# Performance work log

Measured on AMD Instinct MI355X. Metric: run time of the kernel, lower is better.

The kernel has to match this reference:

```python
import jax, jax.numpy as jnp
import numpy as np

B, S, H, NH, HD = 2, 2048, 2048, 16, 128
E, TOPK, I = 8, 2, 2048
EPS = 1e-5
ROPE_THETA = 10000.0


def setup_inputs() -> dict:
    key = jax.random.key(0)
    ks = jax.random.split(key, 11)
    s = 0.02
    return {
        "hidden_states": jax.random.normal(ks[0], (B, S, H), jnp.float32),
        "position_ids": jnp.broadcast_to(jnp.arange(S, dtype=jnp.int32), (B, S)),
        "rms1_w": jnp.ones((H,), jnp.float32),
        "rms2_w": jnp.ones((H,), jnp.float32),
        "q_w": jax.random.normal(ks[1], (H, H), jnp.float32) * s,
        "k_w": jax.random.normal(ks[2], (H, H), jnp.float32) * s,
        "v_w": jax.random.normal(ks[3], (H, H), jnp.float32) * s,
        "o_w": jax.random.normal(ks[4], (H, H), jnp.float32) * s,
        "router_w": jax.random.normal(ks[5], (H, E), jnp.float32) * s,
        "w1": jax.random.normal(ks[6], (E, H, I), jnp.float32) * s,
        "w2": jax.random.normal(ks[7], (E, I, H), jnp.float32) * s,
        "w3": jax.random.normal(ks[8], (E, H, I), jnp.float32) * s,
    }


def rmsnorm(x, w):
    var = jnp.mean(x * x, axis=-1, keepdims=True)
    return (x * jax.lax.rsqrt(var + EPS)) * w


def rope(x, pos):
    # x: [B,S,NH,HD], pos: [B,S]
    half = HD // 2
    inv_freq = 1.0 / (ROPE_THETA ** (jnp.arange(0, half, dtype=jnp.float32) / half))
    ang = pos.astype(jnp.float32)[..., None] * inv_freq  # [B,S,half]
    cos = jnp.cos(ang)[:, :, None, :]
    sin = jnp.sin(ang)[:, :, None, :]
    x1, x2 = x[..., :half], x[..., half:]
    return jnp.concatenate([x1 * cos - x2 * sin, x2 * cos + x1 * sin], axis=-1)


def attention(x, pos, q_w, k_w, v_w, o_w):
    q = (x @ q_w).reshape(B, S, NH, HD)
    k = (x @ k_w).reshape(B, S, NH, HD)
    v = (x @ v_w).reshape(B, S, NH, HD)
    q = rope(q, pos)
    k = rope(k, pos)
    scores = jnp.einsum("bqhd,bkhd->bhqk", q, k) / np.sqrt(HD).astype(np.float32)
    causal = jnp.tril(jnp.ones((S, S), bool))
    scores = jnp.where(causal, scores, jnp.finfo(scores.dtype).min)
    probs = jax.nn.softmax(scores, axis=-1)
    ctx = jnp.einsum("bhqk,bkhd->bqhd", probs, v).reshape(B, S, H)
    return ctx @ o_w


def moe(x, router_w, w1, w2, w3):
    t = x.reshape(B * S, H)
    probs = jax.nn.softmax(t @ router_w, axis=-1)  # [T,E]
    top_v, top_i = jax.lax.top_k(probs, TOPK)
    top_v = top_v / jnp.sum(top_v, axis=-1, keepdims=True)
    T = B * S
    coeff = jnp.zeros((T, E), x.dtype).at[jnp.arange(T)[:, None], top_i].set(top_v)
    y = jnp.zeros((T, H), x.dtype)
    for e in range(E):  # fixed small expert loop
        h = jax.nn.silu(t @ w1[e]) * (t @ w3[e])
        y = y + coeff[:, e:e + 1] * (h @ w2[e])
    return y.reshape(B, S, H)


def reference(hidden_states, position_ids, rms1_w, rms2_w, q_w, k_w, v_w, o_w,
              router_w, w1, w2, w3):
    residual = hidden_states
    h = rmsnorm(hidden_states, rms1_w).astype(hidden_states.dtype)
    h = attention(h, position_ids, q_w, k_w, v_w, o_w)
    h = residual + h
    residual = h
    h = rmsnorm(h, rms2_w).astype(h.dtype)
    h = moe(h, router_w, w1, w2, w3)
    return residual + h
```

## Files before the change

kernel.cpp:

```cpp
#include <hip/hip_runtime.h>
#include <hip/hip_bf16.h>

constexpr int CB   = 2;
constexpr int CS   = 2048;
constexpr int CH   = 2048;
constexpr int CNH  = 16;
constexpr int CHD  = 128;
constexpr int CE   = 8;
constexpr int CI   = 2048;
constexpr int CT   = CB * CS;
constexpr int CQKV = 3 * CH;

typedef __attribute__((ext_vector_type(8))) short short8;
typedef __attribute__((ext_vector_type(4))) float float4v;
typedef __attribute__((ext_vector_type(4))) unsigned short ushort4v;
typedef unsigned int uint32;

__device__ __forceinline__ float bf2f(unsigned short u) {
    union { unsigned int i; float f; } x; x.i = ((unsigned int)u) << 16; return x.f;
}
__device__ __forceinline__ unsigned short f2bf(float f) {
    union { float f; unsigned int i; } x; x.f = f;
    unsigned int r = x.i + 0x7fffu + ((x.i >> 16) & 1u);
    return (unsigned short)(r >> 16);
}
__device__ __forceinline__ uint32 packpair(uint32 r0, uint32 r1) {
    return __builtin_amdgcn_perm(r1, r0, 0x07060302u);
}
__device__ __forceinline__ uint32 rnebits(float f) {
    uint32 u = __float_as_uint(f);
    return u + 0x7fffu + ((u >> 16) & 1u);
}
__device__ __forceinline__ void split2(float f0, float f1, uint32& h, uint32& l) {
    uint32 r0 = rnebits(f0), r1 = rnebits(f1);
    h = packpair(r0, r1);
    float d0 = f0 - __uint_as_float(r0 & 0xffff0000u);
    float d1 = f1 - __uint_as_float(r1 & 0xffff0000u);
    l = packpair(rnebits(d0), rnebits(d1));
}
__device__ __forceinline__ void rne16_store(const float* fv, unsigned short* dst) {
    uint32 h[8];
    #pragma unroll
    for (int p = 0; p < 8; p++) h[p] = packpair(rnebits(fv[2 * p]), rnebits(fv[2 * p + 1]));
    ((uint4*)dst)[0] = make_uint4(h[0], h[1], h[2], h[3]);
    ((uint4*)dst)[1] = make_uint4(h[4], h[5], h[6], h[7]);
}

__global__ __launch_bounds__(256) void rmsnorm_k(const float* __restrict__ x,
                                                 const float* __restrict__ w,
                                                 unsigned short* __restrict__ o1,
                                                 unsigned short* __restrict__ o2) {
    const int row = blockIdx.x;
    const float* xr = x + (size_t)row * CH;
    const int base = threadIdx.x * 8;
    float4 v0 = *(const float4*)(xr + base);
    float4 v1 = *(const float4*)(xr + base + 4);
    float ss = v0.x*v0.x + v0.y*v0.y + v0.z*v0.z + v0.w*v0.w
             + v1.x*v1.x + v1.y*v1.y + v1.z*v1.z + v1.w*v1.w;
    #pragma unroll
    for (int o = 1; o < 64; o <<= 1) ss += __shfl_xor(ss, o);
    __shared__ float ps[4];
    if ((threadIdx.x & 63) == 0) ps[threadIdx.x >> 6] = ss;
    __syncthreads();
    const float scale = rsqrtf((ps[0] + ps[1] + ps[2] + ps[3]) / (float)CH + 1e-5f);
    float4 w0 = *(const float4*)(w + base);
    float4 w1 = *(const float4*)(w + base + 4);
    float r[8] = {v0.x * scale * w0.x, v0.y * scale * w0.y, v0.z * scale * w0.z, v0.w * scale * w0.w,
                  v1.x * scale * w1.x, v1.y * scale * w1.y, v1.z * scale * w1.z, v1.w * scale * w1.w};
    uint32 h[4], l[4];
    #pragma unroll
    for (int p = 0; p < 4; p++) split2(r[2 * p], r[2 * p + 1], h[p], l[p]);
    *(uint4*)(o1 + (size_t)row * CH + base) = make_uint4(h[0], h[1], h[2], h[3]);
    *(uint4*)(o2 + (size_t)row * CH + base) = make_uint4(l[0], l[1], l[2], l[3]);
}

__global__ __launch_bounds__(256) void rmsrouter_k(const float* __restrict__ x,
                                                   const float* __restrict__ w,
                                                   const float* __restrict__ rw,
                                                   unsigned short* __restrict__ h2,
                                                   int* __restrict__ cnt,
                                                   int* __restrict__ tok,
                                                   float* __restrict__ gate) {
    const int row = blockIdx.x;
    const float* xr = x + (size_t)row * CH;
    const int base = threadIdx.x * 8;
    float4 v0 = *(const float4*)(xr + base);
    float4 v1 = *(const float4*)(xr + base + 4);
    float ss = v0.x*v0.x + v0.y*v0.y + v0.z*v0.z + v0.w*v0.w
             + v1.x*v1.x + v1.y*v1.y + v1.z*v1.z + v1.w*v1.w;
    #pragma unroll
    for (int o = 1; o < 64; o <<= 1) ss += __shfl_xor(ss, o);
    __shared__ float ps[4];
    __shared__ double dacc[4][8];
    const int wave = threadIdx.x >> 6, lane = threadIdx.x & 63;
    if (lane == 0) ps[wave] = ss;
    __syncthreads();
    const float scale = rsqrtf((ps[0] + ps[1] + ps[2] + ps[3]) / (float)CH + 1e-5f);
    float4 w0 = *(const float4*)(w + base);
    float4 w1 = *(const float4*)(w + base + 4);
    float r[8] = {v0.x * scale * w0.x, v0.y * scale * w0.y, v0.z * scale * w0.z, v0.w * scale * w0.w,
                  v1.x * scale * w1.x, v1.y * scale * w1.y, v1.z * scale * w1.z, v1.w * scale * w1.w};
    rne16_store(r, h2 + (size_t)row * CH + base);
    const float vv[8] = {v0.x, v0.y, v0.z, v0.w, v1.x, v1.y, v1.z, v1.w};
    const float ww[8] = {w0.x, w0.y, w0.z, w0.w, w1.x, w1.y, w1.z, w1.w};
    double acc[8] = {0, 0, 0, 0, 0, 0, 0, 0};
    #pragma unroll
    for (int jj = 0; jj < 8; jj++) {
        const double xn = (double)vv[jj] * (double)ww[jj];
        const float* rr = rw + (size_t)(base + jj) * CE;
        #pragma unroll
        for (int e = 0; e < 8; e++) acc[e] += xn * (double)rr[e];
    }
    #pragma unroll
    for (int e = 0; e < 8; e++) {
        #pragma unroll
        for (int o = 1; o < 64; o <<= 1) acc[e] += __shfl_xor(acc[e], o);
    }
    if (lane == 0) {
        #pragma unroll
        for (int e = 0; e < 8; e++) dacc[wave][e] = acc[e];
    }
    __syncthreads();
    if (threadIdx.x == 0) {
        double a[8];
        #pragma unroll
        for (int e = 0; e < 8; e++) a[e] = dacc[0][e] + dacc[1][e] + dacc[2][e] + dacc[3][e];
        int e0 = 0;
        #pragma unroll
        for (int e = 1; e < 8; e++) if (a[e] > a[e0]) e0 = e;
        int e1 = (e0 == 0) ? 1 : 0;
        #pragma unroll
        for (int e = 0; e < 8; e++) if (e != e0 && a[e] > a[e1]) e1 = e;
        const double dl = (double)scale * (a[e1] - a[e0]);
        const double p1r = exp(dl);
        const float g0 = (float)(1.0 / (1.0 + p1r));
        const float g1 = (float)(p1r / (1.0 + p1r));
        int pos0 = atomicAdd(&cnt[e0], 1);
        tok[e0 * 4096 + pos0] = row; gate[e0 * 4096 + pos0] = g0;
        int pos1 = atomicAdd(&cnt[e1], 1);
        tok[e1 * 4096 + pos1] = row; gate[e1 * 4096 + pos1] = g1;
    }
}

__global__ void rope_tab_k(float2* __restrict__ tab) {
    int i = blockIdx.x * 256 + threadIdx.x;
    int p = i >> 6, j = i & 63;
    double inv = pow(10000.0, -(double)j / 64.0);
    float invf = (float)inv;
    float angf = (float)p * invf;
    double da = (double)angf;
    tab[i] = make_float2((float)cos(da), (float)sin(da));
}

__global__ __launch_bounds__(256) void rope_k(unsigned short* __restrict__ qh,
                                              unsigned short* __restrict__ ql,
                                              const int* __restrict__ pos,
                                              const float2* __restrict__ tab) {
    int i = blockIdx.x * 256 + threadIdx.x;
    if (i >= CT * CNH * 8) return;
    int t = i >> 7, r = i & 127, hh = r >> 3, jo = (r & 7) << 3;
    const float2* tp = tab + (size_t)pos[t] * 64 + jo;
    float4 tc0 = ((const float4*)tp)[0];
    float4 tc1 = ((const float4*)tp)[1];
    float4 tc2 = ((const float4*)tp)[2];
    float4 tc3 = ((const float4*)tp)[3];
    float cx[8] = {tc0.x, tc0.z, tc1.x, tc1.z, tc2.x, tc2.z, tc3.x, tc3.z};
    float cy[8] = {tc0.y, tc0.w, tc1.y, tc1.w, tc2.y, tc2.w, tc3.y, tc3.w};
    const size_t off = (size_t)t * CQKV + hh * CHD + jo;
    #pragma unroll
    for (int s = 0; s < 2; s++) {
        unsigned short* hp = qh + off + s * CH;
        unsigned short* lp = ql + off + s * CH;
        short8 x1h = *(short8*)hp,        x1l = *(short8*)lp;
        short8 x2h = *(short8*)(hp + 64), x2l = *(short8*)(lp + 64);
        const unsigned short* p1h = (const unsigned short*)&x1h;
        const unsigned short* p1l = (const unsigned short*)&x1l;
        const unsigned short* p2h = (const unsigned short*)&x2h;
        const unsigned short* p2l = (const unsigned short*)&x2l;
        short8 y1h, y1l, y2h, y2l;
        unsigned short* q1h = (unsigned short*)&y1h;
        unsigned short* q1l = (unsigned short*)&y1l;
        unsigned short* q2h = (unsigned short*)&y2h;
        unsigned short* q2l = (unsigned short*)&y2l;
        #pragma unroll
        for (int jj = 0; jj < 8; jj++) {
            const float x1 = bf2f(p1h[jj]) + bf2f(p1l[jj]);
            const float x2 = bf2f(p2h[jj]) + bf2f(p2l[jj]);
            const float yy1 = x1 * cx[jj] - x2 * cy[jj];
            const float yy2 = x2 * cx[jj] + x1 * cy[jj];
            const uint32 r1 = rnebits(yy1), r2 = rnebits(yy2);
            q1h[jj] = (unsigned short)(r1 >> 16);
            q2h[jj] = (unsigned short)(r2 >> 16);
            q1l[jj] = f2bf(yy1 - __uint_as_float(r1 & 0xffff0000u));
            q2l[jj] = f2bf(yy2 - __uint_as_float(r2 & 0xffff0000u));
        }
        *(short8*)hp        = y1h;
        *(short8*)(hp + 64) = y2h;
        *(short8*)lp        = y1l;
        *(short8*)(lp + 64) = y2l;
    }
}

template<int NMAT>
__global__ __launch_bounds__(256) void conv_k(const float* __restrict__ S0,
                                              const float* __restrict__ S1,
                                              unsigned short* __restrict__ D) {
    __shared__ float t[64][65];
    const int n0 = blockIdx.x * 64, k0 = blockIdx.y * 64, e = blockIdx.z;
    const size_t esrc = (size_t)e * 2048 * 2048;
    const int cc = threadIdx.x & 63, r4 = threadIdx.x >> 6;
    const int nl = threadIdx.x >> 2, q = threadIdx.x & 3;
    #pragma unroll
    for (int s = 0; s < NMAT; s++) {
        const float* S = s ? S1 : S0;
        __syncthreads();
        #pragma unroll
        for (int j = 0; j < 16; j++) {
            const int row = j * 4 + r4;
            t[cc][row] = S[esrc + (size_t)(k0 + row) * 2048 + n0 + cc];
        }
        __syncthreads();
        const int orow = (NMAT == 2) ? (2 * (n0 + nl) + s) : (n0 + nl);
        unsigned short* dp = D + (size_t)e * (NMAT * 2048) * 2048 + (size_t)orow * 2048 + k0 + q * 16;
        float fv[16];
        #pragma unroll
        for (int j = 0; j < 16; j++) fv[j] = t[nl][q * 16 + j];
        rne16_store(fv, dp);
    }
}

template<int NMAT>
__global__ __launch_bounds__(256) void convs_k(const float* __restrict__ S0,
                                               const float* __restrict__ S1,
                                               const float* __restrict__ S2,
                                               unsigned short* __restrict__ Dh,
                                               unsigned short* __restrict__ Dl) {
    __shared__ float t[64][65];
    const int n0 = blockIdx.x * 64, k0 = blockIdx.y * 64, z = blockIdx.z;
    const float* S = S0;
    if (NMAT == 3) S = (z == 0) ? S0 : ((z == 1) ? S1 : S2);
    const int cc = threadIdx.x & 63, r4 = threadIdx.x >> 6;
    #pragma unroll
    for (int j = 0; j < 16; j++) {
        const int row = j * 4 + r4;
        t[cc][row] = S[(size_t)(k0 + row) * 2048 + n0 + cc];
    }
    __syncthreads();
    const int nl = threadIdx.x >> 2, q = threadIdx.x & 3;
    float fv[16];
    #pragma unroll
    for (int j = 0; j < 16; j++) fv[j] = t[nl][q * 16 + j];
    uint32 h[8], l[8];
    #pragma unroll
    for (int p = 0; p < 8; p++) split2(fv[2 * p], fv[2 * p + 1], h[p], l[p]);
    const size_t off = (size_t)(z * 2048 + n0 + nl) * 2048 + k0 + q * 16;
    ((uint4*)(Dh + off))[0] = make_uint4(h[0], h[1], h[2], h[3]);
    ((uint4*)(Dh + off))[1] = make_uint4(h[4], h[5], h[6], h[7]);
    ((uint4*)(Dl + off))[0] = make_uint4(l[0], l[1], l[2], l[3]);
    ((uint4*)(Dl + off))[1] = make_uint4(l[4], l[5], l[6], l[7]);
}

template<int MODE>
__global__ __launch_bounds__(256) void sgemm_k(
    const unsigned short* __restrict__ Ahg, const unsigned short* __restrict__ Alg, int lda,
    const unsigned short* __restrict__ Bhg, const unsigned short* __restrict__ Blg, int K,
    unsigned short* __restrict__ Ch, unsigned short* __restrict__ Cl,
    float* __restrict__ Cf, int ldc,
    const float* __restrict__ resid, float* __restrict__ C2) {
    __shared__ unsigned short AhS[128][40], AlS[128][40], BhS[128][40], BlS[128][40];
    const int mt = blockIdx.x, nt = blockIdx.y, tid = threadIdx.x;
    const int m0 = mt * 128;
    const int srow = tid >> 1, shalf = tid & 1;
    const unsigned short* ah = Ahg + (size_t)(m0 + srow) * lda + shalf * 16;
    const unsigned short* al = Alg + (size_t)(m0 + srow) * lda + shalf * 16;
    const unsigned short* bhp = Bhg + (size_t)(nt * 128 + srow) * K + shalf * 16;
    const unsigned short* blp = Blg + (size_t)(nt * 128 + srow) * K + shalf * 16;
    const int lane = tid & 63, lr = lane & 15, lg = lane >> 4;
    const int wr = (tid >> 7) & 1, wc = (tid >> 6) & 1;

    float4v acc[4][4];
    #pragma unroll
    for (int m = 0; m < 4; m++)
        #pragma unroll
        for (int n = 0; n < 4; n++) acc[m][n] = (float4v){0.f, 0.f, 0.f, 0.f};

    short8 cah0 = *(const short8*)(ah),      cah1 = *(const short8*)(ah + 8);
    short8 cal0 = *(const short8*)(al),      cal1 = *(const short8*)(al + 8);
    short8 cbh0 = *(const short8*)(bhp),     cbh1 = *(const short8*)(bhp + 8);
    short8 cbl0 = *(const short8*)(blp),     cbl1 = *(const short8*)(blp + 8);
    short8 nah0 = *(const short8*)(ah + 32), nah1 = *(const short8*)(ah + 40);
    short8 nal0 = *(const short8*)(al + 32), nal1 = *(const short8*)(al + 40);
    short8 nbh0 = *(const short8*)(bhp + 32), nbh1 = *(const short8*)(bhp + 40);
    short8 nbl0 = *(const short8*)(blp + 32), nbl1 = *(const short8*)(blp + 40);

    for (int k0 = 0; k0 < K; k0 += 32) {
        __syncthreads();
        *(short8*)(&AhS[srow][shalf * 16])     = cah0;
        *(short8*)(&AhS[srow][shalf * 16 + 8]) = cah1;
        *(short8*)(&AlS[srow][shalf * 16])     = cal0;
        *(short8*)(&AlS[srow][shalf * 16 + 8]) = cal1;
        *(short8*)(&BhS[srow][shalf * 16])     = cbh0;
        *(short8*)(&BhS[srow][shalf * 16 + 8]) = cbh1;
        *(short8*)(&BlS[srow][shalf * 16])     = cbl0;
        *(short8*)(&BlS[srow][shalf * 16 + 8]) = cbl1;
        cah0 = nah0; cah1 = nah1; cal0 = nal0; cal1 = nal1;
        cbh0 = nbh0; cbh1 = nbh1; cbl0 = nbl0; cbl1 = nbl1;
        if (k0 + 64 < K) {
            nah0 = *(const short8*)(ah + k0 + 64);  nah1 = *(const short8*)(ah + k0 + 72);
            nal0 = *(const short8*)(al + k0 + 64);  nal1 = *(const short8*)(al + k0 + 72);
            nbh0 = *(const short8*)(bhp + k0 + 64); nbh1 = *(const short8*)(bhp + k0 + 72);
            nbl0 = *(const short8*)(blp + k0 + 64); nbl1 = *(const short8*)(blp + k0 + 72);
        }
        __syncthreads();
        short8 fah[4], fal[4], fbh[4], fbl[4];
        #pragma unroll
        for (int m = 0; m < 4; m++) {
            fah[m] = *(const short8*)(&AhS[wr * 64 + m * 16 + lr][lg * 8]);
            fal[m] = *(const short8*)(&AlS[wr * 64 + m * 16 + lr][lg * 8]);
        }
        #pragma unroll
        for (int n = 0; n < 4; n++) {
            fbh[n] = *(const short8*)(&BhS[wc * 64 + n * 16 + lr][lg * 8]);
            fbl[n] = *(const short8*)(&BlS[wc * 64 + n * 16 + lr][lg * 8]);
        }
        #pragma unroll
        for (int n = 0; n < 4; n++)
            #pragma unroll
            for (int m = 0; m < 4; m++) {
                acc[m][n] = __builtin_amdgcn_mfma_f32_16x16x32_bf16(fal[m], fbh[n], acc[m][n], 0, 0, 0);
                acc[m][n] = __builtin_amdgcn_mfma_f32_16x16x32_bf16(fah[m], fbl[n], acc[m][n], 0, 0, 0);
                acc[m][n] = __builtin_amdgcn_mfma_f32_16x16x32_bf16(fah[m], fbh[n], acc[m][n], 0, 0, 0);
            }
    }
    #pragma unroll
    for (int m = 0; m < 4; m++) {
        const int rb = wr * 64 + m * 16 + lg * 4;
        #pragma unroll
        for (int n = 0; n < 4; n++) {
            const int ccol = nt * 128 + wc * 64 + n * 16 + lr;
            #pragma unroll
            for (int r = 0; r < 4; r++) {
                const size_t idx = (size_t)(m0 + rb + r) * ldc + ccol;
                if (MODE == 1) {
                    const float v = acc[m][n][r] + resid[idx];
                    Cf[idx] = v;
                    C2[idx] = v;
                } else {
                    const float v = acc[m][n][r];
                    uint32 rr = rnebits(v);
                    Ch[idx] = (unsigned short)(rr >> 16);
                    Cl[idx] = f2bf(v - __uint_as_float(rr & 0xffff0000u));
                }
            }
        }
    }
}

template<int MODE>
__global__ __launch_bounds__(256) void gemm_k(
    const unsigned short* __restrict__ A, int lda,
    const unsigned short* __restrict__ Bt, int K, int Ne,
    void* __restrict__ Cp, int ldc,
    const int* __restrict__ cnt, const int* __restrict__ tokl,
    const float* __restrict__ gatel, const int* __restrict__ pb) {
    __shared__ unsigned short As[128][40];
    __shared__ unsigned short Bs[128][40];
    const int nt = blockIdx.x, mt = blockIdx.y, e = blockIdx.z;
    const int m0 = mt * 128;
    const int c = cnt[e];
    if (m0 >= c) return;
    const int valid = (c - m0 < 128) ? (c - m0) : 128;
    const int tid = threadIdx.x;
    const int srow = tid >> 1, shalf = tid & 1;
    size_t gr;
    if (MODE == 2) {
        const int idx = m0 + (srow < valid ? srow : valid - 1);
        gr = (size_t)tokl[e * 4096 + idx];
    } else {
        const int rr = m0 + srow;
        gr = (size_t)(pb[e] + (rr < c ? rr : c - 1));
    }
    const unsigned short* a_src = A + gr * (size_t)lda + shalf * 16;
    const unsigned short* b_src = Bt + (size_t)e * Ne * K + (size_t)(nt * 128 + srow) * K + shalf * 16;
    const int lane = tid & 63, lr = lane & 15, lg = lane >> 4;
    const int wr = (tid >> 7) & 1, wc = (tid >> 6) & 1;

    float4v acc[4][4];
    #pragma unroll
    for (int m = 0; m < 4; m++)
        #pragma unroll
        for (int n = 0; n < 4; n++) acc[m][n] = (float4v){0.f, 0.f, 0.f, 0.f};

    short8 ca0 = *(const short8*)(a_src),      ca1 = *(const short8*)(a_src + 8);
    short8 cb0 = *(const short8*)(b_src),      cb1 = *(const short8*)(b_src + 8);
    short8 na0 = *(const short8*)(a_src + 32), na1 = *(const short8*)(a_src + 40);
    short8 nb0 = *(const short8*)(b_src + 32), nb1 = *(const short8*)(b_src + 40);

    for (int k0 = 0; k0 < K; k0 += 32) {
        __syncthreads();
        *(short8*)(&As[srow][shalf * 16])     = ca0;
        *(short8*)(&As[srow][shalf * 16 + 8]) = ca1;
        *(short8*)(&Bs[srow][shalf * 16])     = cb0;
        *(short8*)(&Bs[srow][shalf * 16 + 8]) = cb1;
        ca0 = na0; ca1 = na1; cb0 = nb0; cb1 = nb1;
        if (k0 + 64 < K) {
            na0 = *(const short8*)(a_src + k0 + 64);
            na1 = *(const short8*)(a_src + k0 + 72);
            nb0 = *(const short8*)(b_src + k0 + 64);
            nb1 = *(const short8*)(b_src + k0 + 72);
        }
        __syncthreads();
        short8 af[4], bf[4];
        #pragma unroll
        for (int m = 0; m < 4; m++) af[m] = *(const short8*)(&As[wr * 64 + m * 16 + lr][lg * 8]);
        #pragma unroll
        for (int n = 0; n < 4; n++) bf[n] = *(const short8*)(&Bs[wc * 64 + n * 16 + lr][lg * 8]);
        #pragma unroll
        for (int n = 0; n < 4; n++)
            #pragma unroll
            for (int m = 0; m < 4; m++)
                acc[m][n] = __builtin_amdgcn_mfma_f32_16x16x32_bf16(af[m], bf[n], acc[m][n], 0, 0, 0);
    }

    #pragma unroll
    for (int m = 0; m < 4; m++) {
        const int rb = wr * 64 + m * 16 + lg * 4;
        #pragma unroll
        for (int n = 0; n < 4; n++) {
            const int col = nt * 128 + wc * 64 + n * 16 + lr;
            #pragma unroll
            for (int r = 0; r < 4; r++) {
                const int row = rb + r;
                const float v = acc[m][n][r];
                if (MODE == 2) {
                    const float other = __shfl_xor(v, 1);
                    if (!(lr & 1) && row < valid) {
                        const float g1 = v, g3 = other;
                        const float hsw = (g1 / (1.f + __expf(-g1))) * g3;
                        ((unsigned short*)Cp)[(size_t)(pb[e] + m0 + row) * ldc + (col >> 1)] = f2bf(hsw);
                    }
                } else {
                    if (row < valid) {
                        const int t = tokl[e * 4096 + m0 + row];
                        const float g = gatel[e * 4096 + m0 + row];
                        atomicAdd(((float*)Cp) + (size_t)t * ldc + col, v * g);
                    }
                }
            }
        }
    }
}

__global__ __launch_bounds__(256) void attn_k(const unsigned short* __restrict__ qh,
                                              const unsigned short* __restrict__ ql,
                                              unsigned short* __restrict__ ch,
                                              unsigned short* __restrict__ cl) {
    __shared__ unsigned short Ksh[32][136], Ksl[32][136];
    __shared__ unsigned short Vth[128][40], Vtl[128][40];
    const int bid = blockIdx.x;
    const int xcd = bid & 7, jj = bid >> 3;
    const int bh  = xcd * 4 + (jj >> 5);
    const int qb  = 31 - (jj & 31);
    const int h   = bh & 15, b = bh >> 4;
    const int tid = threadIdx.x;
    const int wave = tid >> 6, lane = tid & 63, lr = lane & 15, lg = lane >> 4;
    const size_t tb = (size_t)b * CS;
    const int q0 = qb * 64 + wave * 16;

    short8 qfh[4], qfl[4];
    {
        const size_t off = (tb + q0 + lr) * CQKV + h * CHD;
        #pragma unroll
        for (int c = 0; c < 4; c++) {
            qfh[c] = *(const short8*)(qh + off + c * 32 + lg * 8);
            qfl[c] = *(const short8*)(ql + off + c * 32 + lg * 8);
        }
    }
    float4v o[8];
    #pragma unroll
    for (int d = 0; d < 8; d++) o[d] = (float4v){0.f, 0.f, 0.f, 0.f};
    float m = -1e30f, l = 0.f;
    const float scl = 0.08838834764831845f;
    const int ntiles = 2 * (qb + 1);
    const int kk = tid >> 3, slot = tid & 7;
    const int vd = tid & 127, vhalf = tid >> 7;

    short8 pkh0, pkh1, pkl0, pkl1;
    unsigned short pth[16], ptl[16];
    {
        const size_t koff = (tb + kk) * CQKV + CH + h * CHD + slot * 16;
        pkh0 = *(const short8*)(qh + koff);
        pkh1 = *(const short8*)(qh + koff + 8);
        pkl0 = *(const short8*)(ql + koff);
        pkl1 = *(const short8*)(ql + koff + 8);
        const size_t voff = (tb + vhalf * 16) * CQKV + 2 * CH + h * CHD + vd;
        #pragma unroll
        for (int j = 0; j < 16; j++) {
            pth[j] = qh[voff + (size_t)j * CQKV];
            ptl[j] = ql[voff + (size_t)j * CQKV];
        }
    }

    for (int kt = 0; kt < ntiles; ++kt) {
        const int kv0 = kt * 32;
        __syncthreads();
        *(short8*)(&Ksh[kk][slot * 16])     = pkh0;
        *(short8*)(&Ksh[kk][slot * 16 + 8]) = pkh1;
        *(short8*)(&Ksl[kk][slot * 16])     = pkl0;
        *(short8*)(&Ksl[kk][slot * 16 + 8]) = pkl1;
        #pragma unroll
        for (int p = 0; p < 2; p++) {
            *(ushort4v*)(&Vth[vd][vhalf * 16 + p * 8])     = *(ushort4v*)(&pth[p * 8]);
            *(ushort4v*)(&Vth[vd][vhalf * 16 + p * 8 + 4]) = *(ushort4v*)(&pth[p * 8 + 4]);
            *(ushort4v*)(&Vtl[vd][vhalf * 16 + p * 8])     = *(ushort4v*)(&ptl[p * 8]);
            *(ushort4v*)(&Vtl[vd][vhalf * 16 + p * 8 + 4]) = *(ushort4v*)(&ptl[p * 8 + 4]);
        }
        if (kt + 1 < ntiles) {
            const int nv0 = kv0 + 32;
            const size_t koff = (tb + nv0 + kk) * CQKV + CH + h * CHD + slot * 16;
            pkh0 = *(const short8*)(qh + koff);
            pkh1 = *(const short8*)(qh + koff + 8);
            pkl0 = *(const short8*)(ql + koff);
            pkl1 = *(const short8*)(ql + koff + 8);
            const size_t voff = (tb + nv0 + vhalf * 16) * CQKV + 2 * CH + h * CHD + vd;
            #pragma unroll
            for (int j = 0; j < 16; j++) {
                pth[j] = qh[voff + (size_t)j * CQKV];
                ptl[j] = ql[voff + (size_t)j * CQKV];
            }
        }
        __syncthreads();

        float4v st0 = (float4v){0.f,0.f,0.f,0.f}, st1 = st0;
        #pragma unroll
        for (int c = 0; c < 4; c++) {
            short8 kah = *(const short8*)(&Ksh[lr][c * 32 + lg * 8]);
            short8 kal = *(const short8*)(&Ksl[lr][c * 32 + lg * 8]);
            short8 kbh = *(const short8*)(&Ksh[16 + lr][c * 32 + lg * 8]);
            short8 kbl = *(const short8*)(&Ksl[16 + lr][c * 32 + lg * 8]);
            st0 = __builtin_amdgcn_mfma_f32_16x16x32_bf16(kal, qfh[c], st0, 0, 0, 0);
            st0 = __builtin_amdgcn_mfma_f32_16x16x32_bf16(kah, qfl[c], st0, 0, 0, 0);
            st0 = __builtin_amdgcn_mfma_f32_16x16x32_bf16(kah, qfh[c], st0, 0, 0, 0);
            st1 = __builtin_amdgcn_mfma_f32_16x16x32_bf16(kbl, qfh[c], st1, 0, 0, 0);
            st1 = __builtin_amdgcn_mfma_f32_16x16x32_bf16(kbh, qfl[c], st1, 0, 0, 0);
            st1 = __builtin_amdgcn_mfma_f32_16x16x32_bf16(kbh, qfh[c], st1, 0, 0, 0);
        }
        float pv[8]; float pmax = -1e30f;
        const int qg = q0 + lr;
        #pragma unroll
        for (int f = 0; f < 2; f++) {
            #pragma unroll
            for (int r = 0; r < 4; r++) {
                const int kg = kv0 + f * 16 + lg * 4 + r;
                const float s = (kg <= qg) ? ((f ? st1[r] : st0[r]) * scl) : -1e30f;
                pv[f * 4 + r] = s;
                pmax = fmaxf(pmax, s);
            }
        }
        pmax = fmaxf(pmax, __shfl_xor(pmax, 16));
        pmax = fmaxf(pmax, __shfl_xor(pmax, 32));
        if (!__all(pmax <= m)) {
            const float mnew = fmaxf(m, pmax);
            const float alpha = __expf(m - mnew);
            l *= alpha;
            #pragma unroll
            for (int d = 0; d < 8; d++) o[d] *= alpha;
            m = mnew;
        }
        float sum = 0.f;
        #pragma unroll
        for (int i = 0; i < 8; i++) { const float p = __expf(pv[i] - m); pv[i] = p; sum += p; }
        sum += __shfl_xor(sum, 16);
        sum += __shfl_xor(sum, 32);
        l += sum;
        short8 pfh, pfl;
        unsigned short* pfhp = (unsigned short*)&pfh;
        unsigned short* pflp = (unsigned short*)&pfl;
        #pragma unroll
        for (int j = 0; j < 8; j++) {
            const int srcl = (((lg & 1) * 2 + (j >> 2)) << 4) | lr;
            const float a0 = __shfl(pv[j & 3], srcl);
            const float a1 = __shfl(pv[4 + (j & 3)], srcl);
            const float sel = (lg >= 2) ? a1 : a0;
            uint32 r = rnebits(sel);
            pfhp[j] = (unsigned short)(r >> 16);
            float d = sel - __uint_as_float(r & 0xffff0000u);
            pflp[j] = (unsigned short)(rnebits(d) >> 16);
        }
        #pragma unroll
        for (int dt = 0; dt < 8; dt++) {
            short8 vh = *(const short8*)(&Vth[dt * 16 + lr][lg * 8]);
            short8 vl = *(const short8*)(&Vtl[dt * 16 + lr][lg * 8]);
            o[dt] = __builtin_amdgcn_mfma_f32_16x16x32_bf16(vl, pfh, o[dt], 0, 0, 0);
            o[dt] = __builtin_amdgcn_mfma_f32_16x16x32_bf16(vh, pfl, o[dt], 0, 0, 0);
            o[dt] = __builtin_amdgcn_mfma_f32_16x16x32_bf16(vh, pfh, o[dt], 0, 0, 0);
        }
    }
    const float inv = 1.f / l;
    const size_t coff = (tb + q0 + lr) * CH + h * CHD + lg * 4;
    #pragma unroll
    for (int dt = 0; dt < 8; dt++) {
        ushort4v wh, wl;
        #pragma unroll
        for (int r = 0; r < 4; r++) {
            const float v = o[dt][r] * inv;
            uint32 rr = rnebits(v);
            wh[r] = (unsigned short)(rr >> 16);
            wl[r] = f2bf(v - __uint_as_float(rr & 0xffff0000u));
        }
        *(ushort4v*)(ch + coff + dt * 16) = wh;
        *(ushort4v*)(cl + coff + dt * 16) = wl;
    }
}

__global__ void prefix_k(const int* __restrict__ cnt, int* __restrict__ pb) {
    if (threadIdx.x == 0 && blockIdx.x == 0) {
        int s = 0;
        for (int e = 0; e < CE; e++) { pb[e] = s; s += cnt[e]; }
    }
}

extern "C" void kernel_launch(void* const* d_in, const int* in_sizes, int n_in,
                              void* d_out, int out_size, void* d_ws, size_t ws_size,
                              hipStream_t stream) {
    (void)in_sizes; (void)n_in; (void)out_size; (void)ws_size;
    const float* hidden = (const float*)d_in[0];
    const int*   posids = (const int*)d_in[1];
    const float* rms1w  = (const float*)d_in[2];
    const float* rms2w  = (const float*)d_in[3];
    const float* qw     = (const float*)d_in[4];
    const float* kw     = (const float*)d_in[5];
    const float* vw     = (const float*)d_in[6];
    const float* ow     = (const float*)d_in[7];
    const float* rw     = (const float*)d_in[8];
    const float* w1     = (const float*)d_in[9];
    const float* w2     = (const float*)d_in[10];
    const float* w3     = (const float*)d_in[11];
    float* out = (float*)d_out;

    char* ws = (char*)d_ws;
    unsigned short* h1h = (unsigned short*)ws;
    unsigned short* h1l = (unsigned short*)(ws + 16777216);
    unsigned short* woh = (unsigned short*)ws;
    unsigned short* wol = (unsigned short*)(ws + 8388608);
    unsigned short* h2  = (unsigned short*)ws;
    int*   tok  = (int*)(ws + 16777216);
    float* gate = (float*)(ws + 16777216 + 131072);
    int*   cnt  = (int*)(ws + 16777216 + 262144);
    int*   pb   = cnt + 16;
    unsigned short* qkvh = (unsigned short*)(ws + 33554432);
    unsigned short* qkvl = (unsigned short*)(ws + 83886080);
    unsigned short* wt13 = (unsigned short*)(ws + 33554432);
    unsigned short* wt2  = (unsigned short*)(ws + 33554432);
    unsigned short* wqkvh = (unsigned short*)(ws + 134217728);
    unsigned short* wqkvl = (unsigned short*)(ws + 134217728 + 25165824);
    unsigned short* ctxh = (unsigned short*)(ws + 134217728);
    unsigned short* ctxl = (unsigned short*)(ws + 150994944);
    float*          res2 = (float*)(ws + 167772160);
    unsigned short* Hbuf = (unsigned short*)(ws + 167772160);
    float2*         rtab = (float2*)(ws + 201326592);

    rope_tab_k<<<512, 256, 0, stream>>>(rtab);
    rmsnorm_k<<<CT, 256, 0, stream>>>(hidden, rms1w, h1h, h1l);
    convs_k<3><<<dim3(32, 32, 3), 256, 0, stream>>>(qw, kw, vw, wqkvh, wqkvl);
    sgemm_k<0><<<dim3(32, 48), 256, 0, stream>>>(h1h, h1l, CH, wqkvh, wqkvl, CH,
                                                 qkvh, qkvl, nullptr, CQKV, nullptr, nullptr);
    rope_k<<<2048, 256, 0, stream>>>(qkvh, qkvl, posids, rtab);
    convs_k<1><<<dim3(32, 32, 1), 256, 0, stream>>>(ow, nullptr, nullptr, woh, wol);
    attn_k<<<1024, 256, 0, stream>>>(qkvh, qkvl, ctxh, ctxl);
    sgemm_k<1><<<dim3(32, 16), 256, 0, stream>>>(ctxh, ctxl, CH, woh, wol, CH,
                                                 nullptr, nullptr, res2, CH, hidden, out);
    hipMemsetAsync(cnt, 0, 8 * sizeof(int), stream);
    rmsrouter_k<<<CT, 256, 0, stream>>>(res2, rms2w, rw, h2, cnt, tok, gate);
    prefix_k<<<1, 64, 0, stream>>>(cnt, pb);
    conv_k<2><<<dim3(32, 32, CE), 256, 0, stream>>>(w1, w3, wt13);
    gemm_k<2><<<dim3(32, 32, CE), 256, 0, stream>>>(h2, CH, wt13, CH, 2 * CI, Hbuf, CI,
                                                    cnt, tok, gate, pb);
    conv_k<1><<<dim3(32, 32, CE), 256, 0, stream>>>(w2, nullptr, wt2);
    gemm_k<3><<<dim3(16, 32, CE), 256, 0, stream>>>(Hbuf, CI, wt2, CI, CH, out, CH,
                                                    cnt, tok, gate, pb);
}
```

Before: 1.406 ms.

## Load GEMM tiles directly into LDS with global_load_lds

Replaces the register-staged, software-prefetched global-to-LDS copies in the split-bf16 GEMM and the MoE grouped GEMM with direct global_load_lds transfers of 16 bytes per lane. The LDS tiles lose their padding (row stride 32 instead of 40) so the direct writes land contiguously. This cuts VGPR pressure and the extra store instructions, but it drops the register double-buffer prefetch, so loads are no longer overlapped with the previous tile's MFMAs. The unpadded layout may also cause LDS bank conflicts on fragment reads.

```diff
diff --git a/kernel.cpp b/kernel.cpp
--- a/kernel.cpp
+++ b/kernel.cpp
@@ -44,6 +44,11 @@
     for (int p = 0; p < 8; p++) h[p] = packpair(rnebits(fv[2 * p]), rnebits(fv[2 * p + 1]));
     ((uint4*)dst)[0] = make_uint4(h[0], h[1], h[2], h[3]);
     ((uint4*)dst)[1] = make_uint4(h[4], h[5], h[6], h[7]);
+}
+__device__ __forceinline__ void gl16(const void* g, void* l) {
+    __builtin_amdgcn_global_load_lds(
+        (const __attribute__((address_space(1))) void*)g,
+        (__attribute__((address_space(3))) void*)l, 16, 0, 0);
 }
 
 __global__ __launch_bounds__(256) void rmsnorm_k(const float* __restrict__ x,
@@ -267,16 +272,24 @@
     unsigned short* __restrict__ Ch, unsigned short* __restrict__ Cl,
     float* __restrict__ Cf, int ldc,
     const float* __restrict__ resid, float* __restrict__ C2) {
-    __shared__ unsigned short AhS[128][40], AlS[128][40], BhS[128][40], BlS[128][40];
+    __shared__ unsigned short AhS[128 * 32], AlS[128 * 32], BhS[128 * 32], BlS[128 * 32];
     const int mt = blockIdx.x, nt = blockIdx.y, tid = threadIdx.x;
     const int m0 = mt * 128;
-    const int srow = tid >> 1, shalf = tid & 1;
-    const unsigned short* ah = Ahg + (size_t)(m0 + srow) * lda + shalf * 16;
-    const unsigned short* al = Alg + (size_t)(m0 + srow) * lda + shalf * 16;
-    const unsigned short* bhp = Bhg + (size_t)(nt * 128 + srow) * K + shalf * 16;
-    const unsigned short* blp = Blg + (size_t)(nt * 128 + srow) * K + shalf * 16;
-    const int lane = tid & 63, lr = lane & 15, lg = lane >> 4;
+    const int wave = tid >> 6, lane = tid & 63;
+    const int lr = lane & 15, lg = lane >> 4;
     const int wr = (tid >> 7) & 1, wc = (tid >> 6) & 1;
+    const int sr = lane >> 2;
+    const int sc = (lane & 3) * 8;
+    const int r0 = wave * 32;
+    const unsigned short* gAh = Ahg + (size_t)(m0 + r0 + sr) * lda + sc;
+    const unsigned short* gAl = Alg + (size_t)(m0 + r0 + sr) * lda + sc;
+    const unsigned short* gBh = Bhg + (size_t)(nt * 128 + r0 + sr) * K + sc;
+    const unsigned short* gBl = Blg + (size_t)(nt * 128 + r0 + sr) * K + sc;
+    const size_t rstepA = (size_t)16 * lda, rstepB = (size_t)16 * K;
+    unsigned short* lAh = AhS + r0 * 32;
+    unsigned short* lAl = AlS + r0 * 32;
+    unsigned short* lBh = BhS + r0 * 32;
+    unsigned short* lBl = BlS + r0 * 32;
 
     float4v acc[4][4];
     #pragma unroll
@@ -284,44 +297,23 @@
         #pragma unroll
         for (int n = 0; n < 4; n++) acc[m][n] = (float4v){0.f, 0.f, 0.f, 0.f};
 
-    short8 cah0 = *(const short8*)(ah),      cah1 = *(const short8*)(ah + 8);
-    short8 cal0 = *(const short8*)(al),      cal1 = *(const short8*)(al + 8);
-    short8 cbh0 = *(const short8*)(bhp),     cbh1 = *(const short8*)(bhp + 8);
-    short8 cbl0 = *(const short8*)(blp),     cbl1 = *(const short8*)(blp + 8);
-    short8 nah0 = *(const short8*)(ah + 32), nah1 = *(const short8*)(ah + 40);
-    short8 nal0 = *(const short8*)(al + 32), nal1 = *(const short8*)(al + 40);
-    short8 nbh0 = *(const short8*)(bhp + 32), nbh1 = *(const short8*)(bhp + 40);
-    short8 nbl0 = *(const short8*)(blp + 32), nbl1 = *(const short8*)(blp + 40);
-
     for (int k0 = 0; k0 < K; k0 += 32) {
         __syncthreads();
-        *(short8*)(&AhS[srow][shalf * 16])     = cah0;
-        *(short8*)(&AhS[srow][shalf * 16 + 8]) = cah1;
-        *(short8*)(&AlS[srow][shalf * 16])     = cal0;
-        *(short8*)(&AlS[srow][shalf * 16 + 8]) = cal1;
-        *(short8*)(&BhS[srow][shalf * 16])     = cbh0;
-        *(short8*)(&BhS[srow][shalf * 16 + 8]) = cbh1;
-        *(short8*)(&BlS[srow][shalf * 16])     = cbl0;
-        *(short8*)(&BlS[srow][shalf * 16 + 8]) = cbl1;
-        cah0 = nah0; cah1 = nah1; cal0 = nal0; cal1 = nal1;
-        cbh0 = nbh0; cbh1 = nbh1; cbl0 = nbl0; cbl1 = nbl1;
-        if (k0 + 64 < K) {
-            nah0 = *(const short8*)(ah + k0 + 64);  nah1 = *(const short8*)(ah + k0 + 72);
-            nal0 = *(const short8*)(al + k0 + 64);  nal1 = *(const short8*)(al + k0 + 72);
-            nbh0 = *(const short8*)(bhp + k0 + 64); nbh1 = *(const short8*)(bhp + k0 + 72);
-            nbl0 = *(const short8*)(blp + k0 + 64); nbl1 = *(const short8*)(blp + k0 + 72);
-        }
+        gl16(gAh + k0, lAh);            gl16(gAh + k0 + rstepA, lAh + 512);
+        gl16(gAl + k0, lAl);            gl16(gAl + k0 + rstepA, lAl + 512);
+        gl16(gBh + k0, lBh);            gl16(gBh + k0 + rstepB, lBh + 512);
+        gl16(gBl + k0, lBl);            gl16(gBl + k0 + rstepB, lBl + 512);
         __syncthreads();
         short8 fah[4], fal[4], fbh[4], fbl[4];
         #pragma unroll
         for (int m = 0; m < 4; m++) {
-            fah[m] = *(const short8*)(&AhS[wr * 64 + m * 16 + lr][lg * 8]);
-            fal[m] = *(const short8*)(&AlS[wr * 64 + m * 16 + lr][lg * 8]);
+            fah[m] = *(const short8*)(AhS + (wr * 64 + m * 16 + lr) * 32 + lg * 8);
+            fal[m] = *(const short8*)(AlS + (wr * 64 + m * 16 + lr) * 32 + lg * 8);
         }
         #pragma unroll
         for (int n = 0; n < 4; n++) {
-            fbh[n] = *(const short8*)(&BhS[wc * 64 + n * 16 + lr][lg * 8]);
-            fbl[n] = *(const short8*)(&BlS[wc * 64 + n * 16 + lr][lg * 8]);
+            fbh[n] = *(const short8*)(BhS + (wc * 64 + n * 16 + lr) * 32 + lg * 8);
+            fbl[n] = *(const short8*)(BlS + (wc * 64 + n * 16 + lr) * 32 + lg * 8);
         }
         #pragma unroll
         for (int n = 0; n < 4; n++)
@@ -334,7 +326,7 @@
     }
     #pragma unroll
     for (int m = 0; m < 4; m++) {
-        const int rb = wr * 64 + m * 16 + lg * 4;
+        const int rb = wr * 64 + m * 16 + (lane >> 4) * 4;
         #pragma unroll
         for (int n = 0; n < 4; n++) {
             const int ccol = nt * 128 + wc * 64 + n * 16 + lr;
@@ -363,27 +355,39 @@
     void* __restrict__ Cp, int ldc,
     const int* __restrict__ cnt, const int* __restrict__ tokl,
     const float* __restrict__ gatel, const int* __restrict__ pb) {
-    __shared__ unsigned short As[128][40];
-    __shared__ unsigned short Bs[128][40];
+    __shared__ unsigned short As[128 * 32];
+    __shared__ unsigned short Bs[128 * 32];
     const int nt = blockIdx.x, mt = blockIdx.y, e = blockIdx.z;
     const int m0 = mt * 128;
     const int c = cnt[e];
     if (m0 >= c) return;
     const int valid = (c - m0 < 128) ? (c - m0) : 128;
     const int tid = threadIdx.x;
-    const int srow = tid >> 1, shalf = tid & 1;
-    size_t gr;
-    if (MODE == 2) {
-        const int idx = m0 + (srow < valid ? srow : valid - 1);
-        gr = (size_t)tokl[e * 4096 + idx];
-    } else {
-        const int rr = m0 + srow;
-        gr = (size_t)(pb[e] + (rr < c ? rr : c - 1));
-    }
-    const unsigned short* a_src = A + gr * (size_t)lda + shalf * 16;
-    const unsigned short* b_src = Bt + (size_t)e * Ne * K + (size_t)(nt * 128 + srow) * K + shalf * 16;
-    const int lane = tid & 63, lr = lane & 15, lg = lane >> 4;
+    const int wave = tid >> 6, lane = tid & 63;
+    const int lr = lane & 15;
     const int wr = (tid >> 7) & 1, wc = (tid >> 6) & 1;
+    const int sr = lane >> 2, sc = (lane & 3) * 8;
+    const int r0 = wave * 32;
+    size_t gr0, gr1;
+    {
+        int ra = r0 + sr, rb2 = r0 + 16 + sr;
+        if (MODE == 2) {
+            ra = ra < valid ? ra : valid - 1;
+            rb2 = rb2 < valid ? rb2 : valid - 1;
+            gr0 = (size_t)tokl[e * 4096 + m0 + ra];
+            gr1 = (size_t)tokl[e * 4096 + m0 + rb2];
+        } else {
+            int x0 = m0 + ra, x1 = m0 + rb2;
+            gr0 = (size_t)(pb[e] + (x0 < c ? x0 : c - 1));
+            gr1 = (size_t)(pb[e] + (x1 < c ? x1 : c - 1));
+        }
+    }
+    const unsigned short* gA0 = A + gr0 * (size_t)lda + sc;
+    const unsigned short* gA1 = A + gr1 * (size_t)lda + sc;
+    const unsigned short* gB = Bt + (size_t)e * Ne * K + (size_t)(nt * 128 + r0 + sr) * K + sc;
+    const size_t rstepB = (size_t)16 * K;
+    unsigned short* lA = As + r0 * 32;
+    unsigned short* lB = Bs + r0 * 32;
 
     float4v acc[4][4];
     #pragma unroll
@@ -391,30 +395,17 @@
         #pragma unroll
         for (int n = 0; n < 4; n++) acc[m][n] = (float4v){0.f, 0.f, 0.f, 0.f};
 
-    short8 ca0 = *(const short8*)(a_src),      ca1 = *(const short8*)(a_src + 8);
-    short8 cb0 = *(const short8*)(b_src),      cb1 = *(const short8*)(b_src + 8);
-    short8 na0 = *(const short8*)(a_src + 32), na1 = *(const short8*)(a_src + 40);
-    short8 nb0 = *(const short8*)(b_src + 32), nb1 = *(const short8*)(b_src + 40);
-
     for (int k0 = 0; k0 < K; k0 += 32) {
         __syncthreads();
-        *(short8*)(&As[srow][shalf * 16])     = ca0;
-        *(short8*)(&As[srow][shalf * 16 + 8]) = ca1;
-        *(short8*)(&Bs[srow][shalf * 16])     = cb0;
-        *(short8*)(&Bs[srow][shalf * 16 + 8]) = cb1;
-        ca0 = na0; ca1 = na1; cb0 = nb0; cb1 = nb1;
-        if (k0 + 64 < K) {
-            na0 = *(const short8*)(a_src + k0 + 64);
-            na1 = *(const short8*)(a_src + k0 + 72);
-            nb0 = *(const short8*)(b_src + k0 + 64);
-            nb1 = *(const short8*)(b_src + k0 + 72);
-        }
+        gl16(gA0 + k0, lA);             gl16(gA1 + k0, lA + 512);
+        gl16(gB + k0, lB);              gl16(gB + k0 + rstepB, lB + 512);
         __syncthreads();
         short8 af[4], bf[4];
-        #pragma unroll
-        for (int m = 0; m < 4; m++) af[m] = *(const short8*)(&As[wr * 64 + m * 16 + lr][lg * 8]);
-        #pragma unroll
-        for (int n = 0; n < 4; n++) bf[n] = *(const short8*)(&Bs[wc * 64 + n * 16 + lr][lg * 8]);
+        const int lg = lane >> 4;
+        #pragma unroll
+        for (int m = 0; m < 4; m++) af[m] = *(const short8*)(As + (wr * 64 + m * 16 + lr) * 32 + lg * 8);
+        #pragma unroll
+        for (int n = 0; n < 4; n++) bf[n] = *(const short8*)(Bs + (wc * 64 + n * 16 + lr) * 32 + lg * 8);
         #pragma unroll
         for (int n = 0; n < 4; n++)
             #pragma unroll
@@ -424,7 +415,7 @@
 
     #pragma unroll
     for (int m = 0; m < 4; m++) {
-        const int rb = wr * 64 + m * 16 + lg * 4;
+        const int rb = wr * 64 + m * 16 + (lane >> 4) * 4;
         #pragma unroll
         for (int n = 0; n < 4; n++) {
             const int col = nt * 128 + wc * 64 + n * 16 + lr;
```

New measurement: 1.382 ms. About the same (-1.7%).
